# Kernel optimization log

Measured on AMD Instinct MI355X. Metric: run time of the kernel, lower is better.

## Reference

```python
import jax, jax.numpy as jnp
import numpy as np

EPS = 1e-08

def setup_inputs() -> dict:
    key = jax.random.key(0)
    ten = jax.random.normal(key, (64, 3, 512, 512), dtype=jnp.float32)
    return {"ten": ten}

def reference(ten):
    # Instance-norm-like: per (n,c) mean and unbiased std over (H,W)
    x = ten.astype(jnp.float32)
    mn = jnp.mean(x, axis=(2, 3), keepdims=True)
    hw = x.shape[2] * x.shape[3]
    var = jnp.sum((x - mn) ** 2, axis=(2, 3), keepdims=True) / (hw - 1)  # unbiased (ddof=1)
    std = jnp.sqrt(var) + EPS
    return (x - mn) / std
```

## Files before the change

kernel.cpp:

```cpp
#include <hip/hip_runtime.h>

#define HW_ELEMS (512 * 512)
#define NC 192
#define EPS 1e-8f

__global__ __launch_bounds__(1024) void instnorm_stats(
    const float* __restrict__ in, float2* __restrict__ stats)
{
    const int c = blockIdx.x;
    const float4* p = reinterpret_cast<const float4*>(in) + (size_t)c * (HW_ELEMS / 4);
    const int t = threadIdx.x;

    float sum = 0.f, sumsq = 0.f;
#pragma unroll
    for (int k = 0; k < HW_ELEMS / 4 / 1024; ++k) {
        float4 v = p[t + k * 1024];
        sum   += (v.x + v.y) + (v.z + v.w);
        sumsq += (v.x * v.x + v.y * v.y) + (v.z * v.z + v.w * v.w);
    }

#pragma unroll
    for (int off = 32; off > 0; off >>= 1) {
        sum   += __shfl_down(sum, off, 64);
        sumsq += __shfl_down(sumsq, off, 64);
    }

    __shared__ float s_sum[16];
    __shared__ float s_sq[16];
    const int wave = t >> 6;
    const int lane = t & 63;
    if (lane == 0) { s_sum[wave] = sum; s_sq[wave] = sumsq; }
    __syncthreads();

    if (t == 0) {
        float S = 0.f, Q = 0.f;
#pragma unroll
        for (int w = 0; w < 16; ++w) { S += s_sum[w]; Q += s_sq[w]; }
        const float n = (float)HW_ELEMS;
        float mean = S / n;
        float var  = (Q - S * S / n) / (n - 1.0f);
        if (var < 0.f) var = 0.f;
        float rstd = 1.0f / (sqrtf(var) + EPS);
        stats[c] = make_float2(mean, rstd);
    }
}

__global__ __launch_bounds__(256) void instnorm_apply(
    const float* __restrict__ in, float* __restrict__ out,
    const float2* __restrict__ stats)
{
    const size_t i4 = (size_t)blockIdx.x * 256 + threadIdx.x;
    const int c = (int)(i4 >> 16);
    const float2 ms = stats[c];
    float4 v = reinterpret_cast<const float4*>(in)[i4];
    float4 r;
    r.x = (v.x - ms.x) * ms.y;
    r.y = (v.y - ms.x) * ms.y;
    r.z = (v.z - ms.x) * ms.y;
    r.w = (v.w - ms.x) * ms.y;
    reinterpret_cast<float4*>(out)[i4] = r;
}

extern "C" void kernel_launch(void* const* d_in, const int* in_sizes, int n_in,
                              void* d_out, int out_size, void* d_ws, size_t ws_size,
                              hipStream_t stream) {
    const float* in = (const float*)d_in[0];
    float* out = (float*)d_out;
    float2* stats = (float2*)d_ws;

    instnorm_stats<<<NC, 1024, 0, stream>>>(in, stats);

    const size_t total4 = (size_t)NC * (HW_ELEMS / 4);
    instnorm_apply<<<(int)(total4 / 256), 256, 0, stream>>>(in, out, stats);
}
```

Before: 97.84 us.

## Split per-channel stats across 8 blocks and finalize stats in apply kernel

Measured after the change: 91.08 us. 1.07x faster.

```diff
diff --git a/kernel.cpp b/kernel.cpp
--- a/kernel.cpp
+++ b/kernel.cpp
@@ -1,20 +1,26 @@
 #include <hip/hip_runtime.h>
 
 #define HW_ELEMS (512 * 512)
+#define HW4      (HW_ELEMS / 4)
 #define NC 192
+#define BPC 8
 #define EPS 1e-8f
 
-__global__ __launch_bounds__(1024) void instnorm_stats(
-    const float* __restrict__ in, float2* __restrict__ stats)
+typedef float fx4 __attribute__((ext_vector_type(4)));
+
+__global__ __launch_bounds__(256) void instnorm_partial(
+    const float* __restrict__ in, float2* __restrict__ partials)
 {
-    const int c = blockIdx.x;
-    const float4* p = reinterpret_cast<const float4*>(in) + (size_t)c * (HW_ELEMS / 4);
+    const int c = blockIdx.x >> 3;
+    const int b = blockIdx.x & (BPC - 1);
+    const fx4* p = reinterpret_cast<const fx4*>(in)
+                 + (size_t)c * HW4 + (size_t)b * (HW4 / BPC);
     const int t = threadIdx.x;
 
     float sum = 0.f, sumsq = 0.f;
 #pragma unroll
-    for (int k = 0; k < HW_ELEMS / 4 / 1024; ++k) {
-        float4 v = p[t + k * 1024];
+    for (int k = 0; k < HW4 / BPC / 256; ++k) {
+        fx4 v = p[t + k * 256];
         sum   += (v.x + v.y) + (v.z + v.w);
         sumsq += (v.x * v.x + v.y * v.y) + (v.z * v.z + v.w * v.w);
     }
@@ -25,40 +31,44 @@
         sumsq += __shfl_down(sumsq, off, 64);
     }
 
-    __shared__ float s_sum[16];
-    __shared__ float s_sq[16];
+    __shared__ float s_sum[4];
+    __shared__ float s_sq[4];
     const int wave = t >> 6;
-    const int lane = t & 63;
-    if (lane == 0) { s_sum[wave] = sum; s_sq[wave] = sumsq; }
+    if ((t & 63) == 0) { s_sum[wave] = sum; s_sq[wave] = sumsq; }
     __syncthreads();
 
     if (t == 0) {
-        float S = 0.f, Q = 0.f;
-#pragma unroll
-        for (int w = 0; w < 16; ++w) { S += s_sum[w]; Q += s_sq[w]; }
-        const float n = (float)HW_ELEMS;
-        float mean = S / n;
-        float var  = (Q - S * S / n) / (n - 1.0f);
-        if (var < 0.f) var = 0.f;
-        float rstd = 1.0f / (sqrtf(var) + EPS);
-        stats[c] = make_float2(mean, rstd);
+        float S = s_sum[0] + s_sum[1] + s_sum[2] + s_sum[3];
+        float Q = s_sq[0] + s_sq[1] + s_sq[2] + s_sq[3];
+        partials[blockIdx.x] = make_float2(S, Q);
     }
 }
 
 __global__ __launch_bounds__(256) void instnorm_apply(
     const float* __restrict__ in, float* __restrict__ out,
-    const float2* __restrict__ stats)
+    const float2* __restrict__ partials)
 {
+    const int c = blockIdx.x >> 8;
+    float S = 0.f, Q = 0.f;
+#pragma unroll
+    for (int b = 0; b < BPC; ++b) {
+        float2 pq = partials[c * BPC + b];
+        S += pq.x; Q += pq.y;
+    }
+    const float n = (float)HW_ELEMS;
+    float mean = S / n;
+    float var  = (Q - S * S / n) / (n - 1.0f);
+    if (var < 0.f) var = 0.f;
+    float rstd = 1.0f / (sqrtf(var) + EPS);
+
     const size_t i4 = (size_t)blockIdx.x * 256 + threadIdx.x;
-    const int c = (int)(i4 >> 16);
-    const float2 ms = stats[c];
-    float4 v = reinterpret_cast<const float4*>(in)[i4];
-    float4 r;
-    r.x = (v.x - ms.x) * ms.y;
-    r.y = (v.y - ms.x) * ms.y;
-    r.z = (v.z - ms.x) * ms.y;
-    r.w = (v.w - ms.x) * ms.y;
-    reinterpret_cast<float4*>(out)[i4] = r;
+    fx4 v = reinterpret_cast<const fx4*>(in)[i4];
+    fx4 r;
+    r.x = (v.x - mean) * rstd;
+    r.y = (v.y - mean) * rstd;
+    r.z = (v.z - mean) * rstd;
+    r.w = (v.w - mean) * rstd;
+    __builtin_nontemporal_store(r, reinterpret_cast<fx4*>(out) + i4);
 }
 
 extern "C" void kernel_launch(void* const* d_in, const int* in_sizes, int n_in,
@@ -66,10 +76,10 @@
                               hipStream_t stream) {
     const float* in = (const float*)d_in[0];
     float* out = (float*)d_out;
-    float2* stats = (float2*)d_ws;
+    float2* partials = (float2*)d_ws;
 
-    instnorm_stats<<<NC, 1024, 0, stream>>>(in, stats);
+    instnorm_partial<<<NC * BPC, 256, 0, stream>>>(in, partials);
 
-    const size_t total4 = (size_t)NC * (HW_ELEMS / 4);
-    instnorm_apply<<<(int)(total4 / 256), 256, 0, stream>>>(in, out, stats);
+    const size_t total4 = (size_t)NC * HW4;
+    instnorm_apply<<<(int)(total4 / 256), 256, 0, stream>>>(in, out, partials);
 }
```
